# Optimization experiments

Measured on AMD Instinct MI355X. Metric: run time of the kernel, lower is better.

Reference implementation:

```python
import jax, jax.numpy as jnp
import numpy as np

BETA = 0.25  # VectorQuantizer commitment beta


def setup_inputs() -> dict:
    key = jax.random.key(0)
    k1, k2, k3, k4 = jax.random.split(key, 4)
    B, T, Zc, D, K = 8, 4096, 512, 256, 8192
    x = jax.random.normal(k1, (B, T, 1, Zc), dtype=jnp.float32)
    W = jax.random.normal(k2, (Zc, D), dtype=jnp.float32) / np.sqrt(Zc)
    b = jax.random.normal(k3, (D,), dtype=jnp.float32) * 0.01
    codebook = jax.random.normal(k4, (K, D), dtype=jnp.float32) / np.sqrt(D)
    return {"x": x, "W": W, "b": b, "codebook": codebook}


def reference(x, W, b, codebook):
    sg = jax.lax.stop_gradient
    # quant_conv: Linear(z_channels -> embed_dim) after squeezing dim 2
    h = jnp.einsum('btc,cd->btd', jnp.squeeze(x, 2), W) + b  # [B,T,D]
    B, T, D = h.shape
    flat = h.reshape(-1, D)  # [B*T, D]
    # squared L2 distances to codebook: ||z||^2 + ||e||^2 - 2 z.e
    d = (jnp.sum(flat * flat, axis=1, keepdims=True)
         + jnp.sum(codebook * codebook, axis=1)
         - 2.0 * flat @ codebook.T)  # [B*T, K]
    idx = jnp.argmin(d, axis=1)  # [B*T]
    zq = jnp.take(codebook, idx, axis=0).reshape(B, T, D)
    # codebook + commitment loss
    emb_loss = (BETA * jnp.mean((sg(zq) - h) ** 2)
                + jnp.mean((zq - sg(h)) ** 2))
    # straight-through estimator
    zq = h + sg(zq - h)
    quant = zq[..., None]  # [B,T,D,1], matching h.unsqueeze(-1) layout
    return quant, emb_loss
```

## Files before the change

kernel.cpp:

```cpp
#include <hip/hip_runtime.h>
#include <stdint.h>

#define M_TOT 32768
#define ZC 512
#define DD 256
#define KCODES 8192
#define NGRAN 512
#define MARGIN 0.15f
#define NBUCKET 256

typedef _Float16 half8   __attribute__((ext_vector_type(8)));
typedef _Float16 half2v  __attribute__((ext_vector_type(2)));
typedef float    float4v __attribute__((ext_vector_type(4)));
typedef float    float16v __attribute__((ext_vector_type(16)));

#define OFF_H     0ull
#define OFF_HT    33554432ull
#define OFF_CBT   50331648ull
#define OFF_HH    54525952ull
#define OFF_EE    54657024ull
#define OFF_LOSSP 54689792ull
#define OFF_SMIN  54691840ull
#define OFF_WTH   OFF_SMIN
#define OFF_WTL   (OFF_SMIN + 524288ull)

#define ASYNC_CP16(gp, lp)                                                     \
  __builtin_amdgcn_global_load_lds(                                            \
      (const __attribute__((address_space(1))) void*)(gp),                     \
      (__attribute__((address_space(3))) void*)(lp), 16, 0, 0)

__global__ __launch_bounds__(256) void k_prep(const float* __restrict__ W,
                                              const float* __restrict__ cb,
                                              _Float16* __restrict__ wt_hi,
                                              _Float16* __restrict__ wt_lo,
                                              _Float16* __restrict__ cbt,
                                              float* __restrict__ ee,
                                              float* __restrict__ loss_part) {
    const int bx = blockIdx.x;
    if (bx < 512) {
        const int idx = bx * 256 + threadIdx.x;
        const int n = idx & 255, k = idx >> 8;
        const float v = W[(size_t)k * DD + n];
        const _Float16 hi = (_Float16)v;
        const _Float16 lo = (_Float16)(v - (float)hi);
        const int off = (((n >> 5) * 64 + (k >> 3)) << 8) + ((n & 31) << 3) + (k & 7);
        wt_hi[off] = hi;
        wt_lo[off] = lo;
        return;
    }
    if (bx == 512) loss_part[threadIdx.x] = 0.0f;
    const int lane = threadIdx.x & 63, w = threadIdx.x >> 6;
    const int code = (bx - 512) * 4 + w;
    float4v v = *(const float4v*)&cb[(size_t)code * DD + lane * 4];
    half2v p0, p1;
    p0.x = (_Float16)v.x; p0.y = (_Float16)v.y;
    p1.x = (_Float16)v.z; p1.y = (_Float16)v.w;
    const size_t off = ((size_t)((code >> 5) * 32 + (lane >> 1)) << 8) +
                       ((code & 31) << 3) + ((lane & 1) << 2);
    *(half2v*)&cbt[off] = p0;
    *(half2v*)&cbt[off + 2] = p1;
    float s = v.x * v.x + v.y * v.y + v.z * v.z + v.w * v.w;
#pragma unroll
    for (int o = 32; o; o >>= 1) s += __shfl_down(s, o);
    if (lane == 0) ee[code] = s;
}

__global__ __launch_bounds__(256) void k_gemm1(const float* __restrict__ x,
                                               const _Float16* __restrict__ wt_hi,
                                               const _Float16* __restrict__ wt_lo,
                                               const float* __restrict__ b,
                                               float* __restrict__ h,
                                               _Float16* __restrict__ ht,
                                               float* __restrict__ hh) {
    __shared__ _Float16 sH[64 * 64];
    __shared__ _Float16 sL[64 * 64];
    __shared__ _Float16 sT[64 * 256];
    __shared__ float sHH[64];
    const int tid = threadIdx.x, lane = tid & 63, w = tid >> 6;
    const int lw = lane & 31, csel = lane >> 5;
    const int wy = w >> 1, wx = w & 1;
    const int m0 = blockIdx.x * 64;

    float16v acc[4];
#pragma unroll
    for (int j = 0; j < 4; ++j) acc[j] = (float16v)(0.0f);

    for (int kb = 0; kb < ZC; kb += 64) {
        __syncthreads();
        {
            const int m = tid & 63;
            const int kp = tid >> 6;
#pragma unroll
            for (int i2 = 0; i2 < 2; ++i2) {
                const int kg = kp * 2 + i2;
                const float* src = x + (size_t)(m0 + m) * ZC + kb + kg * 8;
                float4v v0 = *(const float4v*)src;
                float4v v1 = *(const float4v*)(src + 4);
                half8 hi, lo;
                float vv[8] = {v0.x, v0.y, v0.z, v0.w, v1.x, v1.y, v1.z, v1.w};
#pragma unroll
                for (int j = 0; j < 8; ++j) {
                    hi[j] = (_Float16)vv[j];
                    lo[j] = (_Float16)(vv[j] - (float)hi[j]);
                }
                const int off = (((m >> 5) * 8 + kg) << 8) + ((m & 31) << 3);
                *(half8*)&sH[off] = hi;
                *(half8*)&sL[off] = lo;
            }
        }
        __syncthreads();
#pragma unroll
        for (int s = 0; s < 4; ++s) {
            const int S = (kb >> 4) + s;
            half8 ah = *(const half8*)&sH[((wy * 8 + 2 * s) << 8) + lane * 8];
            half8 al = *(const half8*)&sL[((wy * 8 + 2 * s) << 8) + lane * 8];
#pragma unroll
            for (int nf = 0; nf < 4; ++nf) {
                const int nblk = wx * 4 + nf;
                const size_t boff = ((size_t)(nblk * 64 + 2 * S) << 8) + lane * 8;
                half8 bh = *(const half8*)&wt_hi[boff];
                half8 bl = *(const half8*)&wt_lo[boff];
                acc[nf] = __builtin_amdgcn_mfma_f32_32x32x16_f16(ah, bh, acc[nf], 0, 0, 0);
                acc[nf] = __builtin_amdgcn_mfma_f32_32x32x16_f16(ah, bl, acc[nf], 0, 0, 0);
                acc[nf] = __builtin_amdgcn_mfma_f32_32x32x16_f16(al, bh, acc[nf], 0, 0, 0);
            }
        }
    }
    float bias[4];
#pragma unroll
    for (int nf = 0; nf < 4; ++nf) bias[nf] = b[wx * 128 + nf * 32 + lw];

    float pr[16];
    __syncthreads();
#pragma unroll
    for (int r = 0; r < 16; ++r) {
        const int row = wy * 32 + (r & 3) + 8 * (r >> 2) + 4 * csel;
        float p = 0.f;
#pragma unroll
        for (int nf = 0; nf < 4; ++nf) {
            const int col = wx * 128 + nf * 32 + lw;
            const float v = acc[nf][r] + bias[nf];
            h[(size_t)(m0 + row) * DD + col] = v;
            sT[row * 256 + (col ^ ((row & 7) << 3))] = (_Float16)v;
            p += v * v;
        }
#pragma unroll
        for (int o = 16; o; o >>= 1) p += __shfl_xor(p, o);
        pr[r] = p;
        if (wx == 0 && lw == 0) sHH[row] = p;
    }
    __syncthreads();
    if (wx == 1 && lw == 0) {
#pragma unroll
        for (int r = 0; r < 16; ++r) {
            const int row = wy * 32 + (r & 3) + 8 * (r >> 2) + 4 * csel;
            sHH[row] += pr[r];
        }
    }
    __syncthreads();
#pragma unroll
    for (int i = 0; i < 8; ++i) {
        const int j = tid + i * 256;
        const int c = j >> 5, rr = j & 31;
        const int row = (c >> 5) * 32 + rr, kg = c & 31;
        half8 v = *(const half8*)&sT[row * 256 + ((kg * 8) ^ ((row & 7) << 3))];
        *(half8*)&ht[(size_t)m0 * 256 + (size_t)j * 8] = v;
    }
    if (tid < 64) hh[m0 + tid] = sHH[tid];
}

__global__ __launch_bounds__(256, 2) void k_dist(const _Float16* __restrict__ ht,
                                                 const _Float16* __restrict__ cbt,
                                                 const float* __restrict__ ee,
                                                 _Float16* __restrict__ smin) {
    __shared__ _Float16 sB[2][64 * 256];
    const int tid = threadIdx.x, lane = tid & 63, w = tid >> 6;
    const int lw = lane & 31, csel = lane >> 5;
    const int bx = blockIdx.x;
    const int by = blockIdx.y;

    half8 afr[2][16];
    const size_t lo = (size_t)lane * 8;
#pragma unroll
    for (int mi = 0; mi < 2; ++mi) {
        const _Float16* base = cbt + (size_t)(bx * 8 + w * 2 + mi) * 8192;
#pragma unroll
        for (int s = 0; s < 16; ++s)
            afr[mi][s] = *(const half8*)(base + s * 512 + lo);
    }
    half8 aext[2], bext;
#pragma unroll
    for (int j = 0; j < 8; ++j) bext[j] = (_Float16)0.f;
    if (csel == 0) bext[0] = (_Float16)(-0.5f);
#pragma unroll
    for (int mi = 0; mi < 2; ++mi) {
        const float e = ee[bx * 256 + w * 64 + mi * 32 + lw];
#pragma unroll
        for (int j = 0; j < 8; ++j) aext[mi][j] = (_Float16)0.f;
        if (csel == 0) aext[mi][0] = (_Float16)e;
    }

    const _Float16* hbase = ht + (size_t)by * 1024 * 256 + (size_t)w * 4096 + lane * 8;
#define STAGE_HS(buf, t)                                                       \
    do {                                                                       \
        const _Float16* g_ = hbase + (size_t)(t) * 16384;                      \
        char* l_ = (char*)&sB[(buf)][0] + w * 8192;                            \
        _Pragma("unroll")                                                      \
        for (int i_ = 0; i_ < 8; ++i_)                                         \
            ASYNC_CP16(g_ + i_ * 512, l_ + i_ * 1024);                         \
    } while (0)

#define LDB(sb_, nj_, s_)                                                      \
    (*(const half8*)&(sb_)[(size_t)((((nj_) * 32) + 2 * (s_) + csel) << 8) + lw * 8])

#define EPI(accA, accB, nj_)                                                   \
    do {                                                                       \
        float g0a = (accA)[0], g1a = (accA)[8];                                \
        float g0b = (accB)[0], g1b = (accB)[8];                                \
        _Pragma("unroll")                                                      \
        for (int r = 1; r < 8; ++r) {                                          \
            g0a = fmaxf(g0a, (accA)[r]);  g1a = fmaxf(g1a, (accA)[8 + r]);     \
            g0b = fmaxf(g0b, (accB)[r]);  g1b = fmaxf(g1b, (accB)[8 + r]);     \
        }                                                                      \
        g0a = fmaxf(g0a, __shfl_xor(g0a, 32));                                 \
        g1a = fmaxf(g1a, __shfl_xor(g1a, 32));                                 \
        g0b = fmaxf(g0b, __shfl_xor(g0b, 32));                                 \
        g1b = fmaxf(g1b, __shfl_xor(g1b, 32));                                 \
        if (lane < 32) {                                                       \
            const int row_ = r0_ + (nj_) * 32 + lane;                          \
            const int gb_ = bx * 16 + w * 4;                                   \
            smin[(size_t)(gb_ + 0) * M_TOT + row_] = (_Float16)(-2.f * g0a);   \
            smin[(size_t)(gb_ + 1) * M_TOT + row_] = (_Float16)(-2.f * g1a);   \
            smin[(size_t)(gb_ + 2) * M_TOT + row_] = (_Float16)(-2.f * g0b);   \
            smin[(size_t)(gb_ + 3) * M_TOT + row_] = (_Float16)(-2.f * g1b);   \
        }                                                                      \
    } while (0)

#define COMPUTE_HS(buf, t)                                                     \
    do {                                                                       \
        const int r0_ = by * 1024 + (t) * 64;                                  \
        const _Float16* sb_ = &sB[(buf)][0];                                   \
        float16v A00 = (float16v)(0.f), A01 = (float16v)(0.f);                 \
        float16v A10 = (float16v)(0.f), A11 = (float16v)(0.f);                 \
        __builtin_amdgcn_s_setprio(1);                                         \
        _Pragma("unroll")                                                      \
        for (int s = 0; s < 16; ++s) {                                         \
            half8 bf0 = LDB(sb_, 0, s);                                        \
            half8 bf1 = LDB(sb_, 1, s);                                        \
            A00 = __builtin_amdgcn_mfma_f32_32x32x16_f16(afr[0][s], bf0, A00, 0, 0, 0); \
            A01 = __builtin_amdgcn_mfma_f32_32x32x16_f16(afr[1][s], bf0, A01, 0, 0, 0); \
            A10 = __builtin_amdgcn_mfma_f32_32x32x16_f16(afr[0][s], bf1, A10, 0, 0, 0); \
            A11 = __builtin_amdgcn_mfma_f32_32x32x16_f16(afr[1][s], bf1, A11, 0, 0, 0); \
        }                                                                      \
        A00 = __builtin_amdgcn_mfma_f32_32x32x16_f16(aext[0], bext, A00, 0, 0, 0); \
        A01 = __builtin_amdgcn_mfma_f32_32x32x16_f16(aext[1], bext, A01, 0, 0, 0); \
        A10 = __builtin_amdgcn_mfma_f32_32x32x16_f16(aext[0], bext, A10, 0, 0, 0); \
        A11 = __builtin_amdgcn_mfma_f32_32x32x16_f16(aext[1], bext, A11, 0, 0, 0); \
        __builtin_amdgcn_s_setprio(0);                                         \
        EPI(A00, A01, 0);                                                      \
        EPI(A10, A11, 1);                                                      \
    } while (0)

    STAGE_HS(0, 0);
    STAGE_HS(1, 1);
    asm volatile("s_waitcnt vmcnt(8)" ::: "memory");
    __builtin_amdgcn_s_barrier();
    __builtin_amdgcn_sched_barrier(0);
    COMPUTE_HS(0, 0);
    __builtin_amdgcn_sched_barrier(0);
    __builtin_amdgcn_s_barrier();

#pragma unroll 1
    for (int t = 1; t < 15; ++t) {
        const int cur = t & 1;
        STAGE_HS(cur ^ 1, t + 1);
        asm volatile("s_waitcnt vmcnt(16)" ::: "memory");
        __builtin_amdgcn_s_barrier();
        __builtin_amdgcn_sched_barrier(0);
        COMPUTE_HS(cur, t);
        __builtin_amdgcn_sched_barrier(0);
        __builtin_amdgcn_s_barrier();
    }
    asm volatile("s_waitcnt vmcnt(8)" ::: "memory");
    __builtin_amdgcn_s_barrier();
    __builtin_amdgcn_sched_barrier(0);
    COMPUTE_HS(1, 15);

#undef STAGE_HS
#undef COMPUTE_HS
#undef LDB
#undef EPI
}

__global__ __launch_bounds__(256, 2) void k_select(const float* __restrict__ h,
                                                   const float* __restrict__ cb,
                                                   const float* __restrict__ hh,
                                                   const float* __restrict__ ee,
                                                   const _Float16* __restrict__ smin,
                                                   float* __restrict__ out,
                                                   float* __restrict__ loss_part) {
    __shared__ _Float16 sS[64][512];
    const int t = threadIdx.x, lane = t & 63, w = t >> 6;
    const int r0 = blockIdx.x * 64;

    for (int gi = t; gi < NGRAN; gi += 256) {
        const _Float16* src = smin + (size_t)gi * M_TOT + r0;
#pragma unroll
        for (int c = 0; c < 8; ++c) {
            half8 v = *(const half8*)(src + c * 8);
#pragma unroll
            for (int j = 0; j < 8; ++j) sS[c * 8 + j][gi] = v[j];
        }
    }
    __syncthreads();

    float lossacc = 0.0f;
    for (int i = 0; i < 16; ++i) {
        const int row = r0 + w * 16 + i;
        float4v hv = *(const float4v*)&h[(size_t)row * DD + lane * 4];
        half8 sm = *(const half8*)&sS[w * 16 + i][lane * 8];
        float vmin = 1e30f;
        float sv[8];
#pragma unroll
        for (int j = 0; j < 8; ++j) {
            sv[j] = (float)sm[j];
            vmin = fminf(vmin, sv[j]);
        }
        float m2 = vmin;
#pragma unroll
        for (int o = 32; o; o >>= 1) m2 = fminf(m2, __shfl_xor(m2, o));
        const float thr = m2 + MARGIN;
        unsigned flags = 0;
#pragma unroll
        for (int j = 0; j < 8; ++j)
            if (sv[j] <= thr) flags |= (1u << j);

        unsigned long long act = __ballot(flags != 0);
        unsigned long long bestk = ~0ull;
        const float hhv = hh[row];
        while (act) {
            const int ln = __ffsll((long long)act) - 1;
            act &= act - 1;
            unsigned fl = (unsigned)__shfl((int)flags, ln);
            while (fl) {
                const int j = __ffs(fl) - 1;
                fl &= fl - 1;
                const int g = ln * 8 + j;
#pragma unroll
                for (int c = 0; c < 16; ++c) {
                    const int code = g * 16 + c;
                    float4v cv = *(const float4v*)&cb[(size_t)code * DD + lane * 4];
                    float s = hv.x * cv.x + hv.y * cv.y + hv.z * cv.z + hv.w * cv.w;
#pragma unroll
                    for (int o = 32; o; o >>= 1) s += __shfl_xor(s, o);
                    const float d = (hhv + ee[code]) - 2.0f * s;
                    const unsigned bts = __float_as_uint(d);
                    const unsigned mb =
                        bts ^ (unsigned)(((int)bts >> 31) | 0x80000000);
                    const unsigned long long key =
                        ((unsigned long long)mb << 32) | (unsigned)code;
                    if (key < bestk) bestk = key;
                }
            }
        }
        const unsigned best = (unsigned)(bestk & 0xffffffffull);
        float4v cv = *(const float4v*)&cb[(size_t)best * DD + lane * 4];
        *(float4v*)&out[(size_t)row * DD + lane * 4] = cv;
        const float dx = cv.x - hv.x, dy = cv.y - hv.y;
        const float dz = cv.z - hv.z, dw = cv.w - hv.w;
        lossacc += dx * dx + dy * dy + dz * dz + dw * dw;
    }
#pragma unroll
    for (int o = 32; o; o >>= 1) lossacc += __shfl_xor(lossacc, o);
    if (lane == 0)
        atomicAdd(&loss_part[(blockIdx.x * 4 + w) & (NBUCKET - 1)], lossacc);
}

__global__ __launch_bounds__(256) void k_final(const float* __restrict__ loss_part,
                                               float* __restrict__ out) {
    const int t = threadIdx.x;
    float s = loss_part[t];
#pragma unroll
    for (int off = 32; off; off >>= 1) s += __shfl_down(s, off);
    __shared__ float wsum[4];
    if ((t & 63) == 0) wsum[t >> 6] = s;
    __syncthreads();
    if (t == 0)
        out[0] = 1.25f * ((wsum[0] + wsum[1]) + (wsum[2] + wsum[3]))
                 / (float)(M_TOT * DD);
}

extern "C" void kernel_launch(void* const* d_in, const int* in_sizes, int n_in,
                              void* d_out, int out_size, void* d_ws, size_t ws_size,
                              hipStream_t stream) {
    const float* x  = (const float*)d_in[0];
    const float* W  = (const float*)d_in[1];
    const float* b  = (const float*)d_in[2];
    const float* cb = (const float*)d_in[3];
    float* out = (float*)d_out;

    char* ws = (char*)d_ws;
    float* h        = (float*)(ws + OFF_H);
    _Float16* ht    = (_Float16*)(ws + OFF_HT);
    _Float16* cbt   = (_Float16*)(ws + OFF_CBT);
    _Float16* wt_hi = (_Float16*)(ws + OFF_WTH);
    _Float16* wt_lo = (_Float16*)(ws + OFF_WTL);
    float* hh       = (float*)(ws + OFF_HH);
    float* ee       = (float*)(ws + OFF_EE);
    _Float16* smin  = (_Float16*)(ws + OFF_SMIN);
    float* loss_part = (float*)(ws + OFF_LOSSP);

    hipLaunchKernelGGL(k_prep, dim3(512 + KCODES / 4), dim3(256), 0, stream,
                       W, cb, wt_hi, wt_lo, cbt, ee, loss_part);
    hipLaunchKernelGGL(k_gemm1, dim3(M_TOT / 64), dim3(256), 0, stream,
                       x, wt_hi, wt_lo, b, h, ht, hh);
    hipLaunchKernelGGL(k_dist, dim3(KCODES / 256, M_TOT / 1024), dim3(256),
                       0, stream, ht, cbt, ee, smin);
    hipLaunchKernelGGL(k_select, dim3(M_TOT / 64), dim3(256), 0, stream,
                       h, cb, hh, ee, smin, out, loss_part);
    hipLaunchKernelGGL(k_final, dim3(1), dim3(256), 0, stream,
                       loss_part, out + (size_t)M_TOT * DD);
}
```

Baseline: 354.4 us.

## Retile gemm1 warps over 64x64 output and fuse loss finalize into select

In gemm1, each warp now owns a 64-row by 64-column tile (2x2 MFMA blocks) instead of 32x128. This halves the global B-fragment loads per MFMA and lets each A fragment from shared memory be reused across two column blocks; row norms are summed through a per-warp shared array. The separate k_final launch is removed: k_select keeps a global completion counter, and the last block to finish reduces the loss buckets. This saves a kernel launch but adds a threadfence and an atomic per block.

```diff
diff --git a/kernel.cpp b/kernel.cpp
--- a/kernel.cpp
+++ b/kernel.cpp
@@ -20,6 +20,7 @@
 #define OFF_HH    54525952ull
 #define OFF_EE    54657024ull
 #define OFF_LOSSP 54689792ull
+#define OFF_CNT   54690816ull
 #define OFF_SMIN  54691840ull
 #define OFF_WTH   OFF_SMIN
 #define OFF_WTL   (OFF_SMIN + 524288ull)
@@ -35,7 +36,8 @@
                                               _Float16* __restrict__ wt_lo,
                                               _Float16* __restrict__ cbt,
                                               float* __restrict__ ee,
-                                              float* __restrict__ loss_part) {
+                                              float* __restrict__ loss_part,
+                                              unsigned* __restrict__ cnt) {
     const int bx = blockIdx.x;
     if (bx < 512) {
         const int idx = bx * 256 + threadIdx.x;
@@ -48,7 +50,10 @@
         wt_lo[off] = lo;
         return;
     }
-    if (bx == 512) loss_part[threadIdx.x] = 0.0f;
+    if (bx == 512) {
+        loss_part[threadIdx.x] = 0.0f;
+        if (threadIdx.x == 0) cnt[0] = 0u;
+    }
     const int lane = threadIdx.x & 63, w = threadIdx.x >> 6;
     const int code = (bx - 512) * 4 + w;
     float4v v = *(const float4v*)&cb[(size_t)code * DD + lane * 4];
@@ -75,15 +80,13 @@
     __shared__ _Float16 sH[64 * 64];
     __shared__ _Float16 sL[64 * 64];
     __shared__ _Float16 sT[64 * 256];
-    __shared__ float sHH[64];
+    __shared__ float sHHp[4][64];
     const int tid = threadIdx.x, lane = tid & 63, w = tid >> 6;
     const int lw = lane & 31, csel = lane >> 5;
-    const int wy = w >> 1, wx = w & 1;
     const int m0 = blockIdx.x * 64;
 
-    float16v acc[4];
-#pragma unroll
-    for (int j = 0; j < 4; ++j) acc[j] = (float16v)(0.0f);
+    float16v a00 = (float16v)(0.f), a01 = (float16v)(0.f);
+    float16v a10 = (float16v)(0.f), a11 = (float16v)(0.f);
 
     for (int kb = 0; kb < ZC; kb += 64) {
         __syncthreads();
@@ -112,49 +115,50 @@
 #pragma unroll
         for (int s = 0; s < 4; ++s) {
             const int S = (kb >> 4) + s;
-            half8 ah = *(const half8*)&sH[((wy * 8 + 2 * s) << 8) + lane * 8];
-            half8 al = *(const half8*)&sL[((wy * 8 + 2 * s) << 8) + lane * 8];
-#pragma unroll
-            for (int nf = 0; nf < 4; ++nf) {
-                const int nblk = wx * 4 + nf;
-                const size_t boff = ((size_t)(nblk * 64 + 2 * S) << 8) + lane * 8;
-                half8 bh = *(const half8*)&wt_hi[boff];
-                half8 bl = *(const half8*)&wt_lo[boff];
-                acc[nf] = __builtin_amdgcn_mfma_f32_32x32x16_f16(ah, bh, acc[nf], 0, 0, 0);
-                acc[nf] = __builtin_amdgcn_mfma_f32_32x32x16_f16(ah, bl, acc[nf], 0, 0, 0);
-                acc[nf] = __builtin_amdgcn_mfma_f32_32x32x16_f16(al, bh, acc[nf], 0, 0, 0);
-            }
-        }
-    }
-    float bias[4];
-#pragma unroll
-    for (int nf = 0; nf < 4; ++nf) bias[nf] = b[wx * 128 + nf * 32 + lw];
-
-    float pr[16];
-    __syncthreads();
-#pragma unroll
-    for (int r = 0; r < 16; ++r) {
-        const int row = wy * 32 + (r & 3) + 8 * (r >> 2) + 4 * csel;
-        float p = 0.f;
-#pragma unroll
-        for (int nf = 0; nf < 4; ++nf) {
-            const int col = wx * 128 + nf * 32 + lw;
-            const float v = acc[nf][r] + bias[nf];
-            h[(size_t)(m0 + row) * DD + col] = v;
-            sT[row * 256 + (col ^ ((row & 7) << 3))] = (_Float16)v;
-            p += v * v;
-        }
-#pragma unroll
-        for (int o = 16; o; o >>= 1) p += __shfl_xor(p, o);
-        pr[r] = p;
-        if (wx == 0 && lw == 0) sHH[row] = p;
-    }
-    __syncthreads();
-    if (wx == 1 && lw == 0) {
+            half8 ah0 = *(const half8*)&sH[((2 * s) << 8) + lane * 8];
+            half8 al0 = *(const half8*)&sL[((2 * s) << 8) + lane * 8];
+            half8 ah1 = *(const half8*)&sH[((8 + 2 * s) << 8) + lane * 8];
+            half8 al1 = *(const half8*)&sL[((8 + 2 * s) << 8) + lane * 8];
+            const size_t b0 = ((size_t)((w * 2 + 0) * 64 + 2 * S) << 8) + lane * 8;
+            const size_t b1 = ((size_t)((w * 2 + 1) * 64 + 2 * S) << 8) + lane * 8;
+            half8 bh0 = *(const half8*)&wt_hi[b0];
+            half8 bl0 = *(const half8*)&wt_lo[b0];
+            half8 bh1 = *(const half8*)&wt_hi[b1];
+            half8 bl1 = *(const half8*)&wt_lo[b1];
+            a00 = __builtin_amdgcn_mfma_f32_32x32x16_f16(ah0, bh0, a00, 0, 0, 0);
+            a01 = __builtin_amdgcn_mfma_f32_32x32x16_f16(ah0, bh1, a01, 0, 0, 0);
+            a10 = __builtin_amdgcn_mfma_f32_32x32x16_f16(ah1, bh0, a10, 0, 0, 0);
+            a11 = __builtin_amdgcn_mfma_f32_32x32x16_f16(ah1, bh1, a11, 0, 0, 0);
+            a00 = __builtin_amdgcn_mfma_f32_32x32x16_f16(ah0, bl0, a00, 0, 0, 0);
+            a01 = __builtin_amdgcn_mfma_f32_32x32x16_f16(ah0, bl1, a01, 0, 0, 0);
+            a10 = __builtin_amdgcn_mfma_f32_32x32x16_f16(ah1, bl0, a10, 0, 0, 0);
+            a11 = __builtin_amdgcn_mfma_f32_32x32x16_f16(ah1, bl1, a11, 0, 0, 0);
+            a00 = __builtin_amdgcn_mfma_f32_32x32x16_f16(al0, bh0, a00, 0, 0, 0);
+            a01 = __builtin_amdgcn_mfma_f32_32x32x16_f16(al0, bh1, a01, 0, 0, 0);
+            a10 = __builtin_amdgcn_mfma_f32_32x32x16_f16(al1, bh0, a10, 0, 0, 0);
+            a11 = __builtin_amdgcn_mfma_f32_32x32x16_f16(al1, bh1, a11, 0, 0, 0);
+        }
+    }
+    const float bias0 = b[w * 64 + lw];
+    const float bias1 = b[w * 64 + 32 + lw];
+#pragma unroll
+    for (int mh = 0; mh < 2; ++mh) {
+        const float16v* A0 = mh ? &a10 : &a00;
+        const float16v* A1 = mh ? &a11 : &a01;
 #pragma unroll
         for (int r = 0; r < 16; ++r) {
-            const int row = wy * 32 + (r & 3) + 8 * (r >> 2) + 4 * csel;
-            sHH[row] += pr[r];
+            const int row = mh * 32 + (r & 3) + 8 * (r >> 2) + 4 * csel;
+            const int col0 = w * 64 + lw;
+            const float v0 = (*A0)[r] + bias0;
+            const float v1 = (*A1)[r] + bias1;
+            h[(size_t)(m0 + row) * DD + col0] = v0;
+            h[(size_t)(m0 + row) * DD + col0 + 32] = v1;
+            sT[row * 256 + (col0 ^ ((row & 7) << 3))] = (_Float16)v0;
+            sT[row * 256 + ((col0 + 32) ^ ((row & 7) << 3))] = (_Float16)v1;
+            float p = v0 * v0 + v1 * v1;
+#pragma unroll
+            for (int o = 16; o; o >>= 1) p += __shfl_xor(p, o);
+            if (lw == 0) sHHp[w][row] = p;
         }
     }
     __syncthreads();
@@ -166,7 +170,8 @@
         half8 v = *(const half8*)&sT[row * 256 + ((kg * 8) ^ ((row & 7) << 3))];
         *(half8*)&ht[(size_t)m0 * 256 + (size_t)j * 8] = v;
     }
-    if (tid < 64) hh[m0 + tid] = sHH[tid];
+    if (tid < 64)
+        hh[m0 + tid] = (sHHp[0][tid] + sHHp[1][tid]) + (sHHp[2][tid] + sHHp[3][tid]);
 }
 
 __global__ __launch_bounds__(256, 2) void k_dist(const _Float16* __restrict__ ht,
@@ -298,7 +303,9 @@
                                                    const float* __restrict__ ee,
                                                    const _Float16* __restrict__ smin,
                                                    float* __restrict__ out,
-                                                   float* __restrict__ loss_part) {
+                                                   float* __restrict__ loss_part,
+                                                   unsigned* __restrict__ cnt,
+                                                   float* __restrict__ out_loss) {
     __shared__ _Float16 sS[64][512];
     const int t = threadIdx.x, lane = t & 63, w = t >> 6;
     const int r0 = blockIdx.x * 64;
@@ -374,20 +381,22 @@
     for (int o = 32; o; o >>= 1) lossacc += __shfl_xor(lossacc, o);
     if (lane == 0)
         atomicAdd(&loss_part[(blockIdx.x * 4 + w) & (NBUCKET - 1)], lossacc);
-}
-
-__global__ __launch_bounds__(256) void k_final(const float* __restrict__ loss_part,
-                                               float* __restrict__ out) {
-    const int t = threadIdx.x;
-    float s = loss_part[t];
-#pragma unroll
-    for (int off = 32; off; off >>= 1) s += __shfl_down(s, off);
-    __shared__ float wsum[4];
-    if ((t & 63) == 0) wsum[t >> 6] = s;
+
+    __threadfence();
+    __shared__ unsigned sdone;
+    if (t == 0) sdone = atomicAdd(cnt, 1u);
     __syncthreads();
-    if (t == 0)
-        out[0] = 1.25f * ((wsum[0] + wsum[1]) + (wsum[2] + wsum[3]))
-                 / (float)(M_TOT * DD);
+    if (sdone == gridDim.x - 1) {
+        float s = atomicAdd(&loss_part[t], 0.0f);
+#pragma unroll
+        for (int o = 32; o; o >>= 1) s += __shfl_down(s, o);
+        __shared__ float wsum[4];
+        if ((t & 63) == 0) wsum[t >> 6] = s;
+        __syncthreads();
+        if (t == 0)
+            out_loss[0] = 1.25f * ((wsum[0] + wsum[1]) + (wsum[2] + wsum[3]))
+                          / (float)(M_TOT * DD);
+    }
 }
 
 extern "C" void kernel_launch(void* const* d_in, const int* in_sizes, int n_in,
@@ -409,15 +418,15 @@
     float* ee       = (float*)(ws + OFF_EE);
     _Float16* smin  = (_Float16*)(ws + OFF_SMIN);
     float* loss_part = (float*)(ws + OFF_LOSSP);
+    unsigned* cnt    = (unsigned*)(ws + OFF_CNT);
 
     hipLaunchKernelGGL(k_prep, dim3(512 + KCODES / 4), dim3(256), 0, stream,
-                       W, cb, wt_hi, wt_lo, cbt, ee, loss_part);
+                       W, cb, wt_hi, wt_lo, cbt, ee, loss_part, cnt);
     hipLaunchKernelGGL(k_gemm1, dim3(M_TOT / 64), dim3(256), 0, stream,
                        x, wt_hi, wt_lo, b, h, ht, hh);
     hipLaunchKernelGGL(k_dist, dim3(KCODES / 256, M_TOT / 1024), dim3(256),
                        0, stream, ht, cbt, ee, smin);
     hipLaunchKernelGGL(k_select, dim3(M_TOT / 64), dim3(256), 0, stream,
-                       h, cb, hh, ee, smin, out, loss_part);
-    hipLaunchKernelGGL(k_final, dim3(1), dim3(256), 0, stream,
-                       loss_part, out + (size_t)M_TOT * DD);
+                       h, cb, hh, ee, smin, out, loss_part, cnt,
+                       out + (size_t)M_TOT * DD);
 }
```

New measurement: 400.5 us. 13.0% more time.
